# Performance work log

Hardware: AMD Instinct MI355X
Metric: run time of the kernel (lower is better)

## Reference

```python
import jax, jax.numpy as jnp
import numpy as np

NUM_BINS = 8
TAIL = 3.0
MIN_W = 1e-3
MIN_H = 1e-3
MIN_D = 1e-3


def setup_inputs() -> dict:
    key = jax.random.key(0)
    k1, k2 = jax.random.split(key)
    inputs = jax.random.normal(k1, (8192, 2048), dtype=jnp.float32)
    params = 0.01 * jax.random.normal(k2, (2048, NUM_BINS * 3 - 1), dtype=jnp.float32)
    return {"inputs": inputs, "params": params}


def _rqs(inputs, params):
    # inputs: (B, D); params: (D, 3K-1). Each dim has its own spline (no coupling).
    K = NUM_BINS
    D = params.shape[0]
    uw = params[:, :K]
    uh = params[:, K:2 * K]
    ud = params[:, 2 * K:]  # (D, K-1)

    # pad edge derivatives so that softplus(const) = 1 - min_derivative (linear tails)
    const = float(np.log(np.exp(1.0 - MIN_D) - 1.0))
    ud = jnp.pad(ud, ((0, 0), (1, 1)), constant_values=const)  # (D, K+1)

    widths = MIN_W + (1.0 - MIN_W * K) * jax.nn.softmax(uw, axis=-1)
    cw = jnp.pad(jnp.cumsum(widths, axis=-1), ((0, 0), (1, 0)))  # (D, K+1) in [0,1]
    cw = (2.0 * TAIL) * cw - TAIL
    cw = cw.at[:, 0].set(-TAIL).at[:, -1].set(TAIL)
    widths = cw[:, 1:] - cw[:, :-1]

    heights = MIN_H + (1.0 - MIN_H * K) * jax.nn.softmax(uh, axis=-1)
    ch = jnp.pad(jnp.cumsum(heights, axis=-1), ((0, 0), (1, 0)))
    ch = (2.0 * TAIL) * ch - TAIL
    ch = ch.at[:, 0].set(-TAIL).at[:, -1].set(TAIL)
    heights = ch[:, 1:] - ch[:, :-1]

    derivs = MIN_D + jax.nn.softplus(ud)  # (D, K+1)

    inside = (inputs >= -TAIL) & (inputs <= TAIL)
    x = jnp.clip(inputs, -TAIL, TAIL)

    # searchsorted per element: bin index in [0, K-1], shape (B, D)
    idx = jnp.clip(jnp.sum((x[..., None] >= cw[None, :, :]).astype(jnp.int32), axis=-1) - 1, 0, K - 1)
    d_idx = jnp.arange(D)[None, :]  # broadcasts with (B, D) idx

    icw = cw[d_idx, idx]
    iw = widths[d_idx, idx]
    ich = ch[d_idx, idx]
    ih = heights[d_idx, idx]
    dlo = derivs[d_idx, idx]
    dhi = derivs[d_idx, idx + 1]

    delta = ih / iw
    theta = (x - icw) / iw
    t1m = theta * (1.0 - theta)

    numerator = ih * (delta * theta ** 2 + dlo * t1m)
    denominator = delta + (dlo + dhi - 2.0 * delta) * t1m
    out = ich + numerator / denominator

    deriv_num = delta ** 2 * (dhi * theta ** 2 + 2.0 * delta * t1m + dlo * (1.0 - theta) ** 2)
    logdet = jnp.log(deriv_num) - 2.0 * jnp.log(denominator)

    out = jnp.where(inside, out, inputs)     # identity tails
    logdet = jnp.where(inside, logdet, 0.0)
    return out, logdet


def reference(inputs, params):
    return _rqs(inputs, params)
```

## Files before the change

kernel.cpp:

```cpp
#include <hip/hip_runtime.h>


constexpr int   KBINS = 8;
constexpr float TAILF = 3.0f;
constexpr float MINW  = 0.001f;
constexpr float MINH  = 0.001f;
constexpr float MIND  = 0.001f;
constexpr int   NROWS = 8192;
constexpr int   NDIM  = 2048;
constexpr int   NPAR  = 3 * KBINS - 1;
constexpr int   VEC   = 2;
constexpr int   BLOCK = 256;
constexpr int   DIMS_PER_BLOCK = BLOCK * VEC;
constexpr int   BLOCKS_PER_ROW = NDIM / DIMS_PER_BLOCK;
constexpr int   GROWS = 256;
constexpr int   ROWS_PER_WALK = NROWS / GROWS;

__device__ __forceinline__ float rcp_fast(float x) {
    return __builtin_amdgcn_rcpf(x);
}

__device__ __forceinline__ float softplusf(float x) {
    return fmaxf(x, 0.0f) + log1pf(expf(-fabsf(x)));
}

__device__ __forceinline__ void build_tables(const float* __restrict__ p,
                                             float* cw, float* ch, float* dv,
                                             float edge_deriv) {
    {
        float u[KBINS];
        float m = p[0];
#pragma unroll
        for (int k = 1; k < KBINS; ++k) m = fmaxf(m, p[k]);
        float s = 0.0f;
#pragma unroll
        for (int k = 0; k < KBINS; ++k) { u[k] = expf(p[k] - m); s += u[k]; }
        const float rs = 1.0f / s;
        const float scale = (1.0f - MINW * KBINS) * rs;
        cw[0] = -TAILF;
        float acc = 0.0f;
#pragma unroll
        for (int k = 0; k < KBINS; ++k) {
            acc += MINW + scale * u[k];
            cw[k + 1] = fmaf(2.0f * TAILF, acc, -TAILF);
        }
        cw[KBINS] = TAILF;
    }
    {
        const float* q = p + KBINS;
        float u[KBINS];
        float m = q[0];
#pragma unroll
        for (int k = 1; k < KBINS; ++k) m = fmaxf(m, q[k]);
        float s = 0.0f;
#pragma unroll
        for (int k = 0; k < KBINS; ++k) { u[k] = expf(q[k] - m); s += u[k]; }
        const float rs = 1.0f / s;
        const float scale = (1.0f - MINH * KBINS) * rs;
        ch[0] = -TAILF;
        float acc = 0.0f;
#pragma unroll
        for (int k = 0; k < KBINS; ++k) {
            acc += MINH + scale * u[k];
            ch[k + 1] = fmaf(2.0f * TAILF, acc, -TAILF);
        }
        ch[KBINS] = TAILF;
    }
    dv[0] = edge_deriv;
    dv[KBINS] = edge_deriv;
#pragma unroll
    for (int k = 1; k < KBINS; ++k)
        dv[k] = MIND + softplusf(p[2 * KBINS + k - 1]);
}

__device__ __forceinline__ void rqs_eval(float x,
                                         const float* cw, const float* ch, const float* dv,
                                         float& o, float& ld) {
    const float xi = fminf(fmaxf(x, -TAILF), TAILF);
    float icw = cw[0], ncw = cw[1];
    float ich = ch[0], nch = ch[1];
    float dlo = dv[0], dhi = dv[1];
#pragma unroll
    for (int k = 1; k < KBINS; ++k) {
        const bool c = xi >= cw[k];
        icw = c ? cw[k]     : icw;
        ncw = c ? cw[k + 1] : ncw;
        ich = c ? ch[k]     : ich;
        nch = c ? ch[k + 1] : nch;
        dlo = c ? dv[k]     : dlo;
        dhi = c ? dv[k + 1] : dhi;
    }
    const float iw  = ncw - icw;
    const float ih  = nch - ich;
    const float riw = rcp_fast(iw);
    const float delta = ih * riw;
    const float theta = (xi - icw) * riw;
    const float omt   = 1.0f - theta;
    const float t1m   = theta * omt;
    const float th2   = theta * theta;
    const float num   = ih * fmaf(delta, th2, dlo * t1m);
    const float den   = fmaf(dlo + dhi - 2.0f * delta, t1m, delta);
    const float o_in  = fmaf(num, rcp_fast(den), ich);
    const float dn    = (delta * delta) *
                        fmaf(dhi, th2, fmaf(2.0f * delta, t1m, dlo * (omt * omt)));
    const float ld_in = logf(dn) - 2.0f * logf(den);
    const bool inside = (x >= -TAILF) && (x <= TAILF);
    o  = inside ? o_in : x;
    ld = inside ? ld_in : 0.0f;
}

__global__ __launch_bounds__(BLOCK)
void rqs_kernel(const float* __restrict__ inp,
                const float* __restrict__ params,
                float* __restrict__ out) {
    const int b        = blockIdx.x;
    const int colBlock = b & (BLOCKS_PER_ROW - 1);
    const int rowGroup = b / BLOCKS_PER_ROW;
    const int d0   = colBlock * DIMS_PER_BLOCK + (int)threadIdx.x * VEC;
    const int row0 = rowGroup * ROWS_PER_WALK;

    const float edge_deriv = MIND + softplusf(logf(expf(1.0f - MIND) - 1.0f));

    float cw[VEC][KBINS + 1], ch[VEC][KBINS + 1], dv[VEC][KBINS + 1];
#pragma unroll
    for (int v = 0; v < VEC; ++v)
        build_tables(params + (size_t)(d0 + v) * NPAR, cw[v], ch[v], dv[v], edge_deriv);

    const float2* __restrict__ in2 = (const float2*)inp;
    float2* __restrict__ out2 = (float2*)out;
    float2* __restrict__ ld2  = (float2*)(out + (size_t)NROWS * NDIM);

    size_t idx2 = ((size_t)row0 * NDIM + d0) >> 1;
#pragma unroll 2
    for (int r = 0; r < ROWS_PER_WALK; ++r) {
        const float2 xv = in2[idx2];
        float o0, l0, o1, l1;
        rqs_eval(xv.x, cw[0], ch[0], dv[0], o0, l0);
        rqs_eval(xv.y, cw[1], ch[1], dv[1], o1, l1);
        out2[idx2] = make_float2(o0, o1);
        ld2[idx2]  = make_float2(l0, l1);
        idx2 += NDIM / 2;
    }
}

extern "C" void kernel_launch(void* const* d_in, const int* in_sizes, int n_in,
                              void* d_out, int out_size, void* d_ws, size_t ws_size,
                              hipStream_t stream) {
    const float* inp    = (const float*)d_in[0];
    const float* params = (const float*)d_in[1];
    float* out          = (float*)d_out;
    rqs_kernel<<<BLOCKS_PER_ROW * GROWS, BLOCK, 0, stream>>>(inp, params, out);
}
```

Baseline: 207.9 us.

## Use fast math intrinsics, nontemporal vector I/O, more row groups and occupancy hint

Replaces the accurate expf, logf and log1pf calls with fast intrinsics and merges the two logarithms in the log-determinant into a single log of dn/den². Global loads and stores become nontemporal vector accesses, the number of row groups doubles to spread work over more blocks, the row loop unroll rises to 4, and launch bounds request 8 blocks per CU. The kernel streams memory, so the main aim is cheaper streaming traffic and better latency hiding. In exchange, the fast intrinsics and the fused log lose some precision, and more blocks means the per-dimension tables are rebuilt more often.

New measurement: 341.4 us. +64.3%, slower.

```diff
diff --git a/kernel.cpp b/kernel.cpp
--- a/kernel.cpp
+++ b/kernel.cpp
@@ -13,15 +13,17 @@
 constexpr int   BLOCK = 256;
 constexpr int   DIMS_PER_BLOCK = BLOCK * VEC;
 constexpr int   BLOCKS_PER_ROW = NDIM / DIMS_PER_BLOCK;
-constexpr int   GROWS = 256;
+constexpr int   GROWS = 512;
 constexpr int   ROWS_PER_WALK = NROWS / GROWS;
+
+typedef float v2f __attribute__((ext_vector_type(2)));
 
 __device__ __forceinline__ float rcp_fast(float x) {
     return __builtin_amdgcn_rcpf(x);
 }
 
-__device__ __forceinline__ float softplusf(float x) {
-    return fmaxf(x, 0.0f) + log1pf(expf(-fabsf(x)));
+__device__ __forceinline__ float softplus_fast(float x) {
+    return fmaxf(x, 0.0f) + __logf(1.0f + __expf(-fabsf(x)));
 }
 
 __device__ __forceinline__ void build_tables(const float* __restrict__ p,
@@ -34,9 +36,8 @@
         for (int k = 1; k < KBINS; ++k) m = fmaxf(m, p[k]);
         float s = 0.0f;
 #pragma unroll
-        for (int k = 0; k < KBINS; ++k) { u[k] = expf(p[k] - m); s += u[k]; }
-        const float rs = 1.0f / s;
-        const float scale = (1.0f - MINW * KBINS) * rs;
+        for (int k = 0; k < KBINS; ++k) { u[k] = __expf(p[k] - m); s += u[k]; }
+        const float scale = (1.0f - MINW * KBINS) * rcp_fast(s);
         cw[0] = -TAILF;
         float acc = 0.0f;
 #pragma unroll
@@ -54,9 +55,8 @@
         for (int k = 1; k < KBINS; ++k) m = fmaxf(m, q[k]);
         float s = 0.0f;
 #pragma unroll
-        for (int k = 0; k < KBINS; ++k) { u[k] = expf(q[k] - m); s += u[k]; }
-        const float rs = 1.0f / s;
-        const float scale = (1.0f - MINH * KBINS) * rs;
+        for (int k = 0; k < KBINS; ++k) { u[k] = __expf(q[k] - m); s += u[k]; }
+        const float scale = (1.0f - MINH * KBINS) * rcp_fast(s);
         ch[0] = -TAILF;
         float acc = 0.0f;
 #pragma unroll
@@ -70,7 +70,7 @@
     dv[KBINS] = edge_deriv;
 #pragma unroll
     for (int k = 1; k < KBINS; ++k)
-        dv[k] = MIND + softplusf(p[2 * KBINS + k - 1]);
+        dv[k] = MIND + softplus_fast(p[2 * KBINS + k - 1]);
 }
 
 __device__ __forceinline__ void rqs_eval(float x,
@@ -100,16 +100,17 @@
     const float th2   = theta * theta;
     const float num   = ih * fmaf(delta, th2, dlo * t1m);
     const float den   = fmaf(dlo + dhi - 2.0f * delta, t1m, delta);
-    const float o_in  = fmaf(num, rcp_fast(den), ich);
+    const float rden  = rcp_fast(den);
+    const float o_in  = fmaf(num, rden, ich);
     const float dn    = (delta * delta) *
                         fmaf(dhi, th2, fmaf(2.0f * delta, t1m, dlo * (omt * omt)));
-    const float ld_in = logf(dn) - 2.0f * logf(den);
+    const float ld_in = __logf(dn * rden * rden);
     const bool inside = (x >= -TAILF) && (x <= TAILF);
     o  = inside ? o_in : x;
     ld = inside ? ld_in : 0.0f;
 }
 
-__global__ __launch_bounds__(BLOCK)
+__global__ __launch_bounds__(BLOCK, 8)
 void rqs_kernel(const float* __restrict__ inp,
                 const float* __restrict__ params,
                 float* __restrict__ out) {
@@ -119,26 +120,28 @@
     const int d0   = colBlock * DIMS_PER_BLOCK + (int)threadIdx.x * VEC;
     const int row0 = rowGroup * ROWS_PER_WALK;
 
-    const float edge_deriv = MIND + softplusf(logf(expf(1.0f - MIND) - 1.0f));
+    const float edge_deriv = MIND + softplus_fast(__logf(__expf(1.0f - MIND) - 1.0f));
 
     float cw[VEC][KBINS + 1], ch[VEC][KBINS + 1], dv[VEC][KBINS + 1];
 #pragma unroll
     for (int v = 0; v < VEC; ++v)
         build_tables(params + (size_t)(d0 + v) * NPAR, cw[v], ch[v], dv[v], edge_deriv);
 
-    const float2* __restrict__ in2 = (const float2*)inp;
-    float2* __restrict__ out2 = (float2*)out;
-    float2* __restrict__ ld2  = (float2*)(out + (size_t)NROWS * NDIM);
+    const v2f* __restrict__ in2 = (const v2f*)inp;
+    v2f* __restrict__ out2 = (v2f*)out;
+    v2f* __restrict__ ld2  = (v2f*)(out + (size_t)NROWS * NDIM);
 
     size_t idx2 = ((size_t)row0 * NDIM + d0) >> 1;
-#pragma unroll 2
+#pragma unroll 4
     for (int r = 0; r < ROWS_PER_WALK; ++r) {
-        const float2 xv = in2[idx2];
+        const v2f xv = __builtin_nontemporal_load(&in2[idx2]);
         float o0, l0, o1, l1;
         rqs_eval(xv.x, cw[0], ch[0], dv[0], o0, l0);
         rqs_eval(xv.y, cw[1], ch[1], dv[1], o1, l1);
-        out2[idx2] = make_float2(o0, o1);
-        ld2[idx2]  = make_float2(l0, l1);
+        v2f ov; ov.x = o0; ov.y = o1;
+        v2f lv; lv.x = l0; lv.y = l1;
+        __builtin_nontemporal_store(ov, &out2[idx2]);
+        __builtin_nontemporal_store(lv, &ld2[idx2]);
         idx2 += NDIM / 2;
     }
 }
```
